# Kernel tuning notes

Hardware: AMD Instinct MI355X
Metric: run time of the kernel (lower is better)

Reference implementation:

```python
import jax, jax.numpy as jnp
import numpy as np

NUM_EXPERTS = 4
MLP_RATIO = 4


def setup_inputs() -> dict:
    key = jax.random.key(0)
    k1, k2, k3, k4, k5, k6 = jax.random.split(key, 6)
    B, N, D = 4, 4096, 1024
    OUT = 1024
    H = D * MLP_RATIO
    x = jax.random.normal(k1, (B, N, D), dtype=jnp.float32)
    expert_mask = jax.random.randint(k2, (B, N), 0, NUM_EXPERTS, dtype=jnp.int64)
    w1 = jax.random.normal(k3, (H, D), dtype=jnp.float32) * 0.02
    b1 = jax.random.normal(k4, (H,), dtype=jnp.float32) * 0.02
    w2 = jax.random.normal(k5, (OUT, H), dtype=jnp.float32) * 0.02
    b2 = jax.random.normal(k6, (OUT,), dtype=jnp.float32) * 0.02
    return {"x": x, "expert_mask": expert_mask, "w1": w1, "b1": b1, "w2": w2, "b2": b2}


def reference(x, expert_mask, w1, b1, w2, b2):
    # x: [B, N, D]; expert_mask: [B, N] in [0, NUM_EXPERTS)
    D = x.shape[-1]
    OUT = w2.shape[0]
    E = NUM_EXPERTS
    y = jnp.zeros(x.shape[:-1] + (OUT,), dtype=x.dtype)
    for e in range(E):
        shift = E - 1 - e  # expert E-1 uses full width
        d_in = D >> shift
        d_hid = d_in * MLP_RATIO
        d_out = OUT >> shift
        # nested slice of shared weights
        h = jax.nn.gelu(
            jnp.einsum('bnd,hd->bnh', x[..., :d_in], w1[:d_hid, :d_in]) + b1[:d_hid],
            approximate=False,
        )
        ye = jnp.einsum('bnh,oh->bno', h, w2[:d_out, :d_hid]) + b2[:d_out]
        ye = jnp.pad(ye, ((0, 0), (0, 0), (0, OUT - d_out)))  # zero-fill unused dims
        y = y + jnp.where((expert_mask == e)[..., None], ye, jnp.zeros((), dtype=x.dtype))
    return y
```

## Files before the change

kernel.cpp:

```cpp
#include <hip/hip_runtime.h>
#include <hip/hip_bf16.h>

#define T_TOK 16384
#define DMODEL 1024
#define HDIM 4096
#define OUTD 1024

typedef __attribute__((ext_vector_type(8))) short short8_t;
typedef __attribute__((ext_vector_type(4))) float f32x4;

#define WS_COUNTS_OFF 0
#define WS_HBASE_OFF 64
#define WS_XBASE_OFF 96
#define WS_LIST_OFF 128
#define WS_XC_OFF   ((size_t)1 << 20)
#define WS_W1BF_OFF ((size_t)34 << 20)
#define WS_W2BF_OFF ((size_t)43 << 20)
#define WS_HBUF_OFF ((size_t)52 << 20)

#define W1N (HDIM * DMODEL)
#define W2N (OUTD * HDIM)

__device__ __forceinline__ short f2bf(float f) {
    union { float f; unsigned u; } x; x.f = f;
    unsigned r = x.u + 0x7FFFu + ((x.u >> 16) & 1u);
    return (short)(r >> 16);
}

__device__ __forceinline__ float gelu_fast(float v) {
    float z = fabsf(v) * 0.7071067811865476f;
    float t = __builtin_amdgcn_rcpf(fmaf(0.3275911f, z, 1.0f));
    float poly = t * fmaf(t, fmaf(t, fmaf(t, fmaf(t, 1.061405429f, -1.453152027f),
                                          1.421413741f), -0.284496736f),
                          0.254829592f);
    float e = fmaf(-poly, __expf(-z * z), 1.0f);
    float erfv = copysignf(e, v);
    return 0.5f * v * (1.0f + erfv);
}

__device__ __forceinline__ void conv8(const float* __restrict__ s, short* __restrict__ d) {
    const float4* s4 = (const float4*)s;
    float4 f0 = s4[0], f1 = s4[1];
    short8_t v;
    v[0] = f2bf(f0.x); v[1] = f2bf(f0.y); v[2] = f2bf(f0.z); v[3] = f2bf(f0.w);
    v[4] = f2bf(f1.x); v[5] = f2bf(f1.y); v[6] = f2bf(f1.z); v[7] = f2bf(f1.w);
    *(short8_t*)d = v;
}

__device__ __forceinline__ void gl_lds16(const short* g, short* lds) {
    __builtin_amdgcn_global_load_lds(
        (const __attribute__((address_space(1))) void*)g,
        (__attribute__((address_space(3))) void*)lds, 16, 0, 0);
}

__global__ void k_convert(const float* __restrict__ w1, const float* __restrict__ w2,
                          short* __restrict__ w1bf, short* __restrict__ w2bf) {
    size_t elem = ((size_t)blockIdx.x * blockDim.x + threadIdx.x) * 8;
    if (elem < (size_t)W1N) {
        conv8(w1 + elem, w1bf + elem);
    } else {
        size_t o = elem - W1N; conv8(w2 + o, w2bf + o);
    }
}

__global__ void k_init(int* counts) {
    if (threadIdx.x < 4) counts[threadIdx.x] = 0;
}

__global__ void k_build(const int* __restrict__ mask, int* counts, int* list) {
    __shared__ int hcnt[4], hb[4], hpos[4];
    int tid = threadIdx.x;
    if (tid < 4) hcnt[tid] = 0;
    __syncthreads();
    int t = blockIdx.x * 256 + tid;
    int e = mask[t] & 3;
    atomicAdd(&hcnt[e], 1);
    __syncthreads();
    if (tid < 4) { hb[tid] = atomicAdd(&counts[tid], hcnt[tid]); hpos[tid] = 0; }
    __syncthreads();
    int p = atomicAdd(&hpos[e], 1);
    list[e * T_TOK + hb[e] + p] = t;
}

__global__ void k_bases(const int* counts, unsigned long long* hbase,
                        unsigned long long* xbase) {
    if (threadIdx.x == 0) {
        unsigned long long ha = 0, xa = 0;
        for (int e = 0; e < 4; ++e) {
            hbase[e] = ha; xbase[e] = xa;
            int d_in = 128 << e;
            ha += (unsigned long long)counts[e] * (unsigned long long)(d_in * 4);
            xa += (unsigned long long)counts[e] * (unsigned long long)d_in;
        }
    }
}

__global__ void k_xgather(const float* __restrict__ x, const int* __restrict__ counts,
                          const unsigned long long* __restrict__ xbase,
                          const int* __restrict__ list, short* __restrict__ xc) {
    const int e = blockIdx.y;
    const int d_in = 128 << e;
    const int cnt = counts[e];
    const size_t nel = (size_t)cnt * d_in;
    const int* lst = list + e * T_TOK;
    short* dst = xc + xbase[e];
    for (size_t idx = ((size_t)blockIdx.x * 256 + threadIdx.x) * 8; idx < nel;
         idx += (size_t)gridDim.x * 256 * 8) {
        int row = (int)(idx >> (7 + e));
        int col = (int)(idx & (d_in - 1));
        int tok = lst[row];
        conv8(x + (size_t)tok * DMODEL + col, dst + idx);
    }
}

__global__ void k_zfill(const int* __restrict__ counts, const int* __restrict__ list,
                        float* __restrict__ y) {
    const int e = blockIdx.y;
    const int d_out = 128 << e;
    const int cnt = counts[e];
    const int* lst = list + e * T_TOK;
    const int wv = threadIdx.x >> 6;
    const int lane = threadIdx.x & 63;
    for (int r = blockIdx.x * 4 + wv; r < cnt; r += gridDim.x * 4) {
        float* row = y + (size_t)lst[r] * OUTD;
        for (int c = d_out + lane * 4; c < OUTD; c += 256)
            *(float4*)(row + c) = (float4){0.f, 0.f, 0.f, 0.f};
    }
}

__global__ __launch_bounds__(256) void k_pass1(
    const short* __restrict__ xc, const short* __restrict__ w1bf,
    const float* __restrict__ b1,
    const int* __restrict__ counts, const unsigned long long* __restrict__ hbase,
    const unsigned long long* __restrict__ xbase, short* __restrict__ hbuf)
{
    int by = blockIdx.y;
    int e, nt;
    if (by < 32)      { e = 3; nt = by; }
    else if (by < 48) { e = 2; nt = by - 32; }
    else if (by < 56) { e = 1; nt = by - 48; }
    else              { e = 0; nt = by - 56; }
    const int d_in = 128 << e;
    const int d_hid = d_in * 4;
    const int n0 = nt * 128;
    const int cnt = counts[e];
    const unsigned long long hb = hbase[e];
    const short* xe = xc + xbase[e];

    __shared__ short Ab[64 * 64];
    __shared__ short Bb[128 * 64];

    const int tid = threadIdx.x;
    const int lane = tid & 63;
    const int w = tid >> 6;
    const int l3 = lane >> 3;
    const int ch = lane & 7;
    const int wm = (w & 1) * 32;
    const int wn = (w >> 1) * 64;

    for (int m0 = blockIdx.x * 64; m0 < cnt; m0 += 64 * 64) {
        int rA[2];
#pragma unroll
        for (int j = 0; j < 2; ++j) {
            int rr = m0 + j * 32 + w * 8 + l3;
            rA[j] = (rr >= cnt) ? (cnt - 1) : rr;
        }

        f32x4 acc[2][4];
#pragma unroll
        for (int i = 0; i < 2; ++i)
#pragma unroll
            for (int j = 0; j < 4; ++j)
                acc[i][j] = (f32x4){0.f, 0.f, 0.f, 0.f};

        for (int k0 = 0; k0 < d_in; k0 += 64) {
#pragma unroll
            for (int j = 0; j < 2; ++j) {
                int r = j * 32 + w * 8 + l3;
                gl_lds16(xe + (size_t)rA[j] * d_in + k0 + ((ch ^ (r & 7)) << 3),
                         &Ab[(j * 32 + w * 8) * 64]);
            }
#pragma unroll
            for (int j = 0; j < 4; ++j) {
                int r = j * 32 + w * 8 + l3;
                gl_lds16(w1bf + (size_t)(n0 + r) * DMODEL + k0 + ((ch ^ (r & 7)) << 3),
                         &Bb[(j * 32 + w * 8) * 64]);
            }
            __syncthreads();
#pragma unroll
            for (int kk = 0; kk < 2; ++kk) {
                short8_t af[2], bfr[4];
                const int q = (lane >> 4) + kk * 4;
#pragma unroll
                for (int mt = 0; mt < 2; ++mt) {
                    int row = wm + mt * 16 + (lane & 15);
                    af[mt] = *(const short8_t*)&Ab[((row << 3) | (q ^ (row & 7))) << 3];
                }
#pragma unroll
                for (int ntn = 0; ntn < 4; ++ntn) {
                    int row = wn + ntn * 16 + (lane & 15);
                    bfr[ntn] = *(const short8_t*)&Bb[((row << 3) | (q ^ (row & 7))) << 3];
                }
#pragma unroll
                for (int mt = 0; mt < 2; ++mt)
#pragma unroll
                    for (int ntn = 0; ntn < 4; ++ntn)
                        acc[mt][ntn] = __builtin_amdgcn_mfma_f32_16x16x32_bf16(
                            af[mt], bfr[ntn], acc[mt][ntn], 0, 0, 0);
            }
            __syncthreads();
        }

        const int cl = lane & 15;
        const int qr = lane >> 4;
#pragma unroll
        for (int ntn = 0; ntn < 4; ++ntn) {
            int col = n0 + wn + ntn * 16 + cl;
            float bias = b1[col];
#pragma unroll
            for (int mt = 0; mt < 2; ++mt) {
#pragma unroll
                for (int r = 0; r < 4; ++r) {
                    int row = wm + mt * 16 + qr * 4 + r;
                    if (m0 + row < cnt) {
                        float v = acc[mt][ntn][r] + bias;
                        hbuf[hb + (unsigned long long)(m0 + row) * d_hid + col] =
                            f2bf(gelu_fast(v));
                    }
                }
            }
        }
    }
}

__global__ __launch_bounds__(256) void k_pass2(
    const short* __restrict__ hbuf, const short* __restrict__ w2bf,
    const float* __restrict__ b2,
    const int* __restrict__ counts, const unsigned long long* __restrict__ hbase,
    const int* __restrict__ list, float* __restrict__ y)
{
    int by = blockIdx.y;
    int e, nt;
    if (by < 8)       { e = 3; nt = by; }
    else if (by < 12) { e = 2; nt = by - 8; }
    else if (by < 14) { e = 1; nt = by - 12; }
    else              { e = 0; nt = 0; }
    const int d_in = 128 << e;
    const int d_hid = d_in * 4;
    const int n0 = nt * 128;
    const int cnt = counts[e];
    const int* lst = list + e * T_TOK;
    const unsigned long long hb = hbase[e];

    __shared__ short Ab[2 * 64 * 64];
    __shared__ short Bb[2 * 128 * 64];

    const int tid = threadIdx.x;
    const int lane = tid & 63;
    const int w = tid >> 6;
    const int l3 = lane >> 3;
    const int ch = lane & 7;
    const int wm = (w & 1) * 32;
    const int wn = (w >> 1) * 64;

    for (int m0 = blockIdx.x * 64; m0 < cnt; m0 += 64 * 64) {
        int rA[2];
#pragma unroll
        for (int j = 0; j < 2; ++j) {
            int rr = m0 + j * 32 + w * 8 + l3;
            rA[j] = (rr >= cnt) ? (cnt - 1) : rr;
        }

        f32x4 acc[2][4];
#pragma unroll
        for (int i = 0; i < 2; ++i)
#pragma unroll
            for (int j = 0; j < 4; ++j)
                acc[i][j] = (f32x4){0.f, 0.f, 0.f, 0.f};

        const int ks = d_hid >> 6;
#pragma unroll
        for (int j = 0; j < 2; ++j) {
            int r = j * 32 + w * 8 + l3;
            gl_lds16(hbuf + hb + (size_t)rA[j] * d_hid + ((ch ^ (r & 7)) << 3),
                     &Ab[(j * 32 + w * 8) * 64]);
        }
#pragma unroll
        for (int j = 0; j < 4; ++j) {
            int r = j * 32 + w * 8 + l3;
            gl_lds16(w2bf + (size_t)(n0 + r) * HDIM + ((ch ^ (r & 7)) << 3),
                     &Bb[(j * 32 + w * 8) * 64]);
        }
        for (int kt = 0; kt < ks; ++kt) {
            const int p = kt & 1;
            __syncthreads();
            if (kt + 1 < ks) {
                const int kn = (kt + 1) << 6;
                const int qb = 1 - p;
#pragma unroll
                for (int j = 0; j < 2; ++j) {
                    int r = j * 32 + w * 8 + l3;
                    gl_lds16(hbuf + hb + (size_t)rA[j] * d_hid + kn + ((ch ^ (r & 7)) << 3),
                             &Ab[(qb * 4096) + (j * 32 + w * 8) * 64]);
                }
#pragma unroll
                for (int j = 0; j < 4; ++j) {
                    int r = j * 32 + w * 8 + l3;
                    gl_lds16(w2bf + (size_t)(n0 + r) * HDIM + kn + ((ch ^ (r & 7)) << 3),
                             &Bb[(qb * 8192) + (j * 32 + w * 8) * 64]);
                }
            }
            const short* Ap = &Ab[p * 4096];
            const short* Bp = &Bb[p * 8192];
#pragma unroll
            for (int kk = 0; kk < 2; ++kk) {
                short8_t af[2], bfr[4];
                const int q = (lane >> 4) + kk * 4;
#pragma unroll
                for (int mt = 0; mt < 2; ++mt) {
                    int row = wm + mt * 16 + (lane & 15);
                    af[mt] = *(const short8_t*)&Ap[((row << 3) | (q ^ (row & 7))) << 3];
                }
#pragma unroll
                for (int ntn = 0; ntn < 4; ++ntn) {
                    int row = wn + ntn * 16 + (lane & 15);
                    bfr[ntn] = *(const short8_t*)&Bp[((row << 3) | (q ^ (row & 7))) << 3];
                }
#pragma unroll
                for (int mt = 0; mt < 2; ++mt)
#pragma unroll
                    for (int ntn = 0; ntn < 4; ++ntn)
                        acc[mt][ntn] = __builtin_amdgcn_mfma_f32_16x16x32_bf16(
                            af[mt], bfr[ntn], acc[mt][ntn], 0, 0, 0);
            }
        }
        __syncthreads();

        const int cl = lane & 15;
        const int qr = lane >> 4;
#pragma unroll
        for (int ntn = 0; ntn < 4; ++ntn) {
            int col = n0 + wn + ntn * 16 + cl;
            float bias = b2[col];
#pragma unroll
            for (int mt = 0; mt < 2; ++mt) {
#pragma unroll
                for (int r = 0; r < 4; ++r) {
                    int row = wm + mt * 16 + qr * 4 + r;
                    if (m0 + row < cnt) {
                        int tok = lst[m0 + row];
                        y[(size_t)tok * OUTD + col] = acc[mt][ntn][r] + bias;
                    }
                }
            }
        }
    }
}

extern "C" void kernel_launch(void* const* d_in, const int* in_sizes, int n_in,
                              void* d_out, int out_size, void* d_ws, size_t ws_size,
                              hipStream_t stream) {
    const float* x  = (const float*)d_in[0];
    const int* mask = (const int*)d_in[1];
    const float* w1 = (const float*)d_in[2];
    const float* b1 = (const float*)d_in[3];
    const float* w2 = (const float*)d_in[4];
    const float* b2 = (const float*)d_in[5];
    float* y = (float*)d_out;

    char* ws = (char*)d_ws;
    int* counts = (int*)(ws + WS_COUNTS_OFF);
    unsigned long long* hbase = (unsigned long long*)(ws + WS_HBASE_OFF);
    unsigned long long* xbase = (unsigned long long*)(ws + WS_XBASE_OFF);
    int* list = (int*)(ws + WS_LIST_OFF);
    short* xc   = (short*)(ws + WS_XC_OFF);
    short* w1bf = (short*)(ws + WS_W1BF_OFF);
    short* w2bf = (short*)(ws + WS_W2BF_OFF);
    short* hbuf = (short*)(ws + WS_HBUF_OFF);

    k_convert<<<(W1N + W2N) / 8 / 256, 256, 0, stream>>>(w1, w2, w1bf, w2bf);

    k_init<<<1, 64, 0, stream>>>(counts);
    k_build<<<T_TOK / 256, 256, 0, stream>>>(mask, counts, list);
    k_bases<<<1, 1, 0, stream>>>(counts, hbase, xbase);
    k_xgather<<<dim3(128, 4), 256, 0, stream>>>(x, counts, xbase, list, xc);

    k_zfill<<<dim3(256, 3), 256, 0, stream>>>(counts, list, y);

    k_pass1<<<dim3(64, 60), 256, 0, stream>>>(xc, w1bf, b1, counts, hbase, xbase, hbuf);
    k_pass2<<<dim3(64, 15), 256, 0, stream>>>(hbuf, w2bf, b2, counts, hbase, list, y);
}
```

Before: 377.1 us.

## Double-buffer pass1 loads, merge tiny setup kernels, relax pipeline barriers

Pass1 moves from single-buffered LDS staging to double buffering, so the next K tile is prefetched while MFMAs run on the current one. Both GEMM passes now use raw s_barrier with an explicit vmcnt wait instead of __syncthreads. Three launches go away: counts init is folded into the weight conversion, the bases kernel is replaced by computing offsets inline, and zero-fill is merged into the gather kernel. This cuts launch overhead and load-latency stalls, but doubles pass1's LDS footprint and depends on hand-written waitcnt values being correct.

```diff
diff --git a/kernel.cpp b/kernel.cpp
--- a/kernel.cpp
+++ b/kernel.cpp
@@ -10,8 +10,6 @@
 typedef __attribute__((ext_vector_type(4))) float f32x4;
 
 #define WS_COUNTS_OFF 0
-#define WS_HBASE_OFF 64
-#define WS_XBASE_OFF 96
 #define WS_LIST_OFF 128
 #define WS_XC_OFF   ((size_t)1 << 20)
 #define WS_W1BF_OFF ((size_t)34 << 20)
@@ -53,18 +51,29 @@
         (__attribute__((address_space(3))) void*)lds, 16, 0, 0);
 }
 
+__device__ __forceinline__ void bases_for(const int* __restrict__ counts, int e,
+                                          unsigned long long* hb,
+                                          unsigned long long* xb) {
+    unsigned long long h = 0, x = 0;
+    for (int i = 0; i < e; ++i) {
+        unsigned long long c = (unsigned long long)counts[i];
+        int din = 128 << i;
+        x += c * (unsigned long long)din;
+        h += c * (unsigned long long)(din * 4);
+    }
+    *hb = h; *xb = x;
+}
+
 __global__ void k_convert(const float* __restrict__ w1, const float* __restrict__ w2,
-                          short* __restrict__ w1bf, short* __restrict__ w2bf) {
+                          short* __restrict__ w1bf, short* __restrict__ w2bf,
+                          int* counts) {
+    if (blockIdx.x == 0 && threadIdx.x < 4) counts[threadIdx.x] = 0;
     size_t elem = ((size_t)blockIdx.x * blockDim.x + threadIdx.x) * 8;
     if (elem < (size_t)W1N) {
         conv8(w1 + elem, w1bf + elem);
     } else {
         size_t o = elem - W1N; conv8(w2 + o, w2bf + o);
     }
-}
-
-__global__ void k_init(int* counts) {
-    if (threadIdx.x < 4) counts[threadIdx.x] = 0;
 }
 
 __global__ void k_build(const int* __restrict__ mask, int* counts, int* list) {
@@ -82,57 +91,44 @@
     list[e * T_TOK + hb[e] + p] = t;
 }
 
-__global__ void k_bases(const int* counts, unsigned long long* hbase,
-                        unsigned long long* xbase) {
-    if (threadIdx.x == 0) {
-        unsigned long long ha = 0, xa = 0;
-        for (int e = 0; e < 4; ++e) {
-            hbase[e] = ha; xbase[e] = xa;
-            int d_in = 128 << e;
-            ha += (unsigned long long)counts[e] * (unsigned long long)(d_in * 4);
-            xa += (unsigned long long)counts[e] * (unsigned long long)d_in;
-        }
-    }
-}
-
 __global__ void k_xgather(const float* __restrict__ x, const int* __restrict__ counts,
-                          const unsigned long long* __restrict__ xbase,
-                          const int* __restrict__ list, short* __restrict__ xc) {
-    const int e = blockIdx.y;
-    const int d_in = 128 << e;
-    const int cnt = counts[e];
-    const size_t nel = (size_t)cnt * d_in;
-    const int* lst = list + e * T_TOK;
-    short* dst = xc + xbase[e];
-    for (size_t idx = ((size_t)blockIdx.x * 256 + threadIdx.x) * 8; idx < nel;
-         idx += (size_t)gridDim.x * 256 * 8) {
-        int row = (int)(idx >> (7 + e));
-        int col = (int)(idx & (d_in - 1));
-        int tok = lst[row];
-        conv8(x + (size_t)tok * DMODEL + col, dst + idx);
-    }
-}
-
-__global__ void k_zfill(const int* __restrict__ counts, const int* __restrict__ list,
-                        float* __restrict__ y) {
-    const int e = blockIdx.y;
-    const int d_out = 128 << e;
-    const int cnt = counts[e];
-    const int* lst = list + e * T_TOK;
-    const int wv = threadIdx.x >> 6;
-    const int lane = threadIdx.x & 63;
-    for (int r = blockIdx.x * 4 + wv; r < cnt; r += gridDim.x * 4) {
-        float* row = y + (size_t)lst[r] * OUTD;
-        for (int c = d_out + lane * 4; c < OUTD; c += 256)
-            *(float4*)(row + c) = (float4){0.f, 0.f, 0.f, 0.f};
+                          const int* __restrict__ list, short* __restrict__ xc,
+                          float* __restrict__ y) {
+    if (blockIdx.y < 4) {
+        const int e = blockIdx.y;
+        const int d_in = 128 << e;
+        const int cnt = counts[e];
+        unsigned long long hbD, xb;
+        bases_for(counts, e, &hbD, &xb);
+        const size_t nel = (size_t)cnt * d_in;
+        const int* lst = list + e * T_TOK;
+        short* dst = xc + xb;
+        for (size_t idx = ((size_t)blockIdx.x * 256 + threadIdx.x) * 8; idx < nel;
+             idx += (size_t)gridDim.x * 256 * 8) {
+            int row = (int)(idx >> (7 + e));
+            int col = (int)(idx & (d_in - 1));
+            int tok = lst[row];
+            conv8(x + (size_t)tok * DMODEL + col, dst + idx);
+        }
+    } else {
+        const int e = blockIdx.y - 4;
+        const int d_out = 128 << e;
+        const int cnt = counts[e];
+        const int* lst = list + e * T_TOK;
+        const int wv = threadIdx.x >> 6;
+        const int lane = threadIdx.x & 63;
+        for (int r = blockIdx.x * 4 + wv; r < cnt; r += gridDim.x * 4) {
+            float* row = y + (size_t)lst[r] * OUTD;
+            for (int c = d_out + lane * 4; c < OUTD; c += 256)
+                *(float4*)(row + c) = (float4){0.f, 0.f, 0.f, 0.f};
+        }
     }
 }
 
 __global__ __launch_bounds__(256) void k_pass1(
     const short* __restrict__ xc, const short* __restrict__ w1bf,
-    const float* __restrict__ b1,
-    const int* __restrict__ counts, const unsigned long long* __restrict__ hbase,
-    const unsigned long long* __restrict__ xbase, short* __restrict__ hbuf)
+    const float* __restrict__ b1, const int* __restrict__ counts,
+    short* __restrict__ hbuf)
 {
     int by = blockIdx.y;
     int e, nt;
@@ -144,11 +140,12 @@
     const int d_hid = d_in * 4;
     const int n0 = nt * 128;
     const int cnt = counts[e];
-    const unsigned long long hb = hbase[e];
-    const short* xe = xc + xbase[e];
-
-    __shared__ short Ab[64 * 64];
-    __shared__ short Bb[128 * 64];
+    unsigned long long hb, xb;
+    bases_for(counts, e, &hb, &xb);
+    const short* xe = xc + xb;
+
+    __shared__ short Ab[2 * 64 * 64];
+    __shared__ short Bb[2 * 128 * 64];
 
     const int tid = threadIdx.x;
     const int lane = tid & 63;
@@ -158,6 +155,17 @@
     const int wm = (w & 1) * 32;
     const int wn = (w >> 1) * 64;
 
+#define P1_STAGE(kn, b) do {                                                   \
+    _Pragma("unroll") for (int j = 0; j < 2; ++j) {                            \
+        int r = j * 32 + w * 8 + l3;                                           \
+        gl_lds16(xe + (size_t)rA[j] * d_in + (kn) + ((ch ^ (r & 7)) << 3),     \
+                 &Ab[(b) * 4096 + (j * 32 + w * 8) * 64]); }                   \
+    _Pragma("unroll") for (int j = 0; j < 4; ++j) {                            \
+        int r = j * 32 + w * 8 + l3;                                           \
+        gl_lds16(w1bf + (size_t)(n0 + r) * DMODEL + (kn) + ((ch ^ (r & 7)) << 3), \
+                 &Bb[(b) * 8192 + (j * 32 + w * 8) * 64]); }                   \
+} while (0)
+
     for (int m0 = blockIdx.x * 64; m0 < cnt; m0 += 64 * 64) {
         int rA[2];
 #pragma unroll
@@ -173,20 +181,20 @@
             for (int j = 0; j < 4; ++j)
                 acc[i][j] = (f32x4){0.f, 0.f, 0.f, 0.f};
 
-        for (int k0 = 0; k0 < d_in; k0 += 64) {
-#pragma unroll
-            for (int j = 0; j < 2; ++j) {
-                int r = j * 32 + w * 8 + l3;
-                gl_lds16(xe + (size_t)rA[j] * d_in + k0 + ((ch ^ (r & 7)) << 3),
-                         &Ab[(j * 32 + w * 8) * 64]);
-            }
-#pragma unroll
-            for (int j = 0; j < 4; ++j) {
-                int r = j * 32 + w * 8 + l3;
-                gl_lds16(w1bf + (size_t)(n0 + r) * DMODEL + k0 + ((ch ^ (r & 7)) << 3),
-                         &Bb[(j * 32 + w * 8) * 64]);
-            }
-            __syncthreads();
+        const int ks = d_in >> 6;
+        P1_STAGE(0, 0);
+        for (int kt = 0; kt < ks; ++kt) {
+            const int p = kt & 1;
+            __builtin_amdgcn_s_barrier();
+            if (kt + 1 < ks) {
+                P1_STAGE((kt + 1) << 6, 1 - p);
+                asm volatile("s_waitcnt vmcnt(6)" ::: "memory");
+            } else {
+                asm volatile("s_waitcnt vmcnt(0)" ::: "memory");
+            }
+            __builtin_amdgcn_s_barrier();
+            const short* Ap = &Ab[p * 4096];
+            const short* Bp = &Bb[p * 8192];
 #pragma unroll
             for (int kk = 0; kk < 2; ++kk) {
                 short8_t af[2], bfr[4];
@@ -194,12 +202,12 @@
 #pragma unroll
                 for (int mt = 0; mt < 2; ++mt) {
                     int row = wm + mt * 16 + (lane & 15);
-                    af[mt] = *(const short8_t*)&Ab[((row << 3) | (q ^ (row & 7))) << 3];
+                    af[mt] = *(const short8_t*)&Ap[((row << 3) | (q ^ (row & 7))) << 3];
                 }
 #pragma unroll
                 for (int ntn = 0; ntn < 4; ++ntn) {
                     int row = wn + ntn * 16 + (lane & 15);
-                    bfr[ntn] = *(const short8_t*)&Bb[((row << 3) | (q ^ (row & 7))) << 3];
+                    bfr[ntn] = *(const short8_t*)&Bp[((row << 3) | (q ^ (row & 7))) << 3];
                 }
 #pragma unroll
                 for (int mt = 0; mt < 2; ++mt)
@@ -208,7 +216,6 @@
                         acc[mt][ntn] = __builtin_amdgcn_mfma_f32_16x16x32_bf16(
                             af[mt], bfr[ntn], acc[mt][ntn], 0, 0, 0);
             }
-            __syncthreads();
         }
 
         const int cl = lane & 15;
@@ -231,12 +238,12 @@
             }
         }
     }
+#undef P1_STAGE
 }
 
 __global__ __launch_bounds__(256) void k_pass2(
     const short* __restrict__ hbuf, const short* __restrict__ w2bf,
-    const float* __restrict__ b2,
-    const int* __restrict__ counts, const unsigned long long* __restrict__ hbase,
+    const float* __restrict__ b2, const int* __restrict__ counts,
     const int* __restrict__ list, float* __restrict__ y)
 {
     int by = blockIdx.y;
@@ -250,7 +257,8 @@
     const int n0 = nt * 128;
     const int cnt = counts[e];
     const int* lst = list + e * T_TOK;
-    const unsigned long long hb = hbase[e];
+    unsigned long long hb, xb;
+    bases_for(counts, e, &hb, &xb);
 
     __shared__ short Ab[2 * 64 * 64];
     __shared__ short Bb[2 * 128 * 64];
@@ -263,6 +271,17 @@
     const int wm = (w & 1) * 32;
     const int wn = (w >> 1) * 64;
 
+#define P2_STAGE(kn, b) do {                                                   \
+    _Pragma("unroll") for (int j = 0; j < 2; ++j) {                            \
+        int r = j * 32 + w * 8 + l3;                                           \
+        gl_lds16(hbuf + hb + (size_t)rA[j] * d_hid + (kn) + ((ch ^ (r & 7)) << 3), \
+                 &Ab[(b) * 4096 + (j * 32 + w * 8) * 64]); }                   \
+    _Pragma("unroll") for (int j = 0; j < 4; ++j) {                            \
+        int r = j * 32 + w * 8 + l3;                                           \
+        gl_lds16(w2bf + (size_t)(n0 + r) * HDIM + (kn) + ((ch ^ (r & 7)) << 3), \
+                 &Bb[(b) * 8192 + (j * 32 + w * 8) * 64]); }                   \
+} while (0)
+
     for (int m0 = blockIdx.x * 64; m0 < cnt; m0 += 64 * 64) {
         int rA[2];
 #pragma unroll
@@ -279,37 +298,17 @@
                 acc[i][j] = (f32x4){0.f, 0.f, 0.f, 0.f};
 
         const int ks = d_hid >> 6;
-#pragma unroll
-        for (int j = 0; j < 2; ++j) {
-            int r = j * 32 + w * 8 + l3;
-            gl_lds16(hbuf + hb + (size_t)rA[j] * d_hid + ((ch ^ (r & 7)) << 3),
-                     &Ab[(j * 32 + w * 8) * 64]);
-        }
-#pragma unroll
-        for (int j = 0; j < 4; ++j) {
-            int r = j * 32 + w * 8 + l3;
-            gl_lds16(w2bf + (size_t)(n0 + r) * HDIM + ((ch ^ (r & 7)) << 3),
-                     &Bb[(j * 32 + w * 8) * 64]);
-        }
+        P2_STAGE(0, 0);
         for (int kt = 0; kt < ks; ++kt) {
             const int p = kt & 1;
-            __syncthreads();
+            __builtin_amdgcn_s_barrier();
             if (kt + 1 < ks) {
-                const int kn = (kt + 1) << 6;
-                const int qb = 1 - p;
-#pragma unroll
-                for (int j = 0; j < 2; ++j) {
-                    int r = j * 32 + w * 8 + l3;
-                    gl_lds16(hbuf + hb + (size_t)rA[j] * d_hid + kn + ((ch ^ (r & 7)) << 3),
-                             &Ab[(qb * 4096) + (j * 32 + w * 8) * 64]);
-                }
-#pragma unroll
-                for (int j = 0; j < 4; ++j) {
-                    int r = j * 32 + w * 8 + l3;
-                    gl_lds16(w2bf + (size_t)(n0 + r) * HDIM + kn + ((ch ^ (r & 7)) << 3),
-                             &Bb[(qb * 8192) + (j * 32 + w * 8) * 64]);
-                }
-            }
+                P2_STAGE((kt + 1) << 6, 1 - p);
+                asm volatile("s_waitcnt vmcnt(6)" ::: "memory");
+            } else {
+                asm volatile("s_waitcnt vmcnt(0)" ::: "memory");
+            }
+            __builtin_amdgcn_s_barrier();
             const short* Ap = &Ab[p * 4096];
             const short* Bp = &Bb[p * 8192];
 #pragma unroll
@@ -334,7 +333,6 @@
                             af[mt], bfr[ntn], acc[mt][ntn], 0, 0, 0);
             }
         }
-        __syncthreads();
 
         const int cl = lane & 15;
         const int qr = lane >> 4;
@@ -355,6 +353,7 @@
             }
         }
     }
+#undef P2_STAGE
 }
 
 extern "C" void kernel_launch(void* const* d_in, const int* in_sizes, int n_in,
@@ -370,23 +369,15 @@
 
     char* ws = (char*)d_ws;
     int* counts = (int*)(ws + WS_COUNTS_OFF);
-    unsigned long long* hbase = (unsigned long long*)(ws + WS_HBASE_OFF);
-    unsigned long long* xbase = (unsigned long long*)(ws + WS_XBASE_OFF);
     int* list = (int*)(ws + WS_LIST_OFF);
     short* xc   = (short*)(ws + WS_XC_OFF);
     short* w1bf = (short*)(ws + WS_W1BF_OFF);
     short* w2bf = (short*)(ws + WS_W2BF_OFF);
     short* hbuf = (short*)(ws + WS_HBUF_OFF);
 
-    k_convert<<<(W1N + W2N) / 8 / 256, 256, 0, stream>>>(w1, w2, w1bf, w2bf);
-
-    k_init<<<1, 64, 0, stream>>>(counts);
+    k_convert<<<(W1N + W2N) / 8 / 256, 256, 0, stream>>>(w1, w2, w1bf, w2bf, counts);
     k_build<<<T_TOK / 256, 256, 0, stream>>>(mask, counts, list);
-    k_bases<<<1, 1, 0, stream>>>(counts, hbase, xbase);
-    k_xgather<<<dim3(128, 4), 256, 0, stream>>>(x, counts, xbase, list, xc);
-
-    k_zfill<<<dim3(256, 3), 256, 0, stream>>>(counts, list, y);
-
-    k_pass1<<<dim3(64, 60), 256, 0, stream>>>(xc, w1bf, b1, counts, hbase, xbase, hbuf);
-    k_pass2<<<dim3(64, 15), 256, 0, stream>>>(hbuf, w2bf, b2, counts, hbase, list, y);
-}
+    k_xgather<<<dim3(128, 7), 256, 0, stream>>>(x, counts, list, xc, y);
+    k_pass1<<<dim3(64, 60), 256, 0, stream>>>(xc, w1bf, b1, counts, hbuf);
+    k_pass2<<<dim3(64, 15), 256, 0, stream>>>(hbuf, w2bf, b2, counts, list, y);
+}
```

Measured after the change: 386.3 us. +2.5%, slower.
